# Optimization experiments

Measured on AMD Instinct MI355X. Metric: run time of the kernel, lower is better.

The kernel has to match this reference:

```python
import jax, jax.numpy as jnp
import numpy as np

B, S, D, H, E = 8, 4096, 1024, 2048, 8


def setup_inputs() -> dict:
    key = jax.random.key(0)
    ks = jax.random.split(key, 7)
    scale = 0.02
    return {
        "x": jax.random.normal(ks[0], (B, S, D), dtype=jnp.float32),
        "W1": jax.random.normal(ks[1], (E, D, H), dtype=jnp.float32) * scale,
        "b1": jnp.zeros((E, H), dtype=jnp.float32),
        "W2": jax.random.normal(ks[2], (E, H, D), dtype=jnp.float32) * scale,
        "b2": jnp.zeros((E, D), dtype=jnp.float32),
        "Wg": jax.random.normal(ks[3], (D, E), dtype=jnp.float32) * scale,
        "bg": jnp.zeros((E,), dtype=jnp.float32),
    }


def reference(x, W1, b1, W2, b2, Wg, bg):
    # Gating: softmax then top-1 (argmax) routing.
    logits = jnp.einsum("bsd,de->bse", x, Wg) + bg          # [B,S,E]
    probs = jax.nn.softmax(logits, axis=-1)                    # [B,S,E]
    top1 = jnp.argmax(probs, axis=-1)                          # [B,S] int

    out = jnp.zeros_like(x)
    # Fixed, small expert count: loop over experts (jit-friendly, no dynamic
    # shapes). coef zeros out tokens not routed to expert e, matching the
    # masked scatter in the original (unrouted positions stay 0 -> impossible
    # with top-1 over all experts, but semantics are identical).
    for e in range(E):
        coef = jnp.where(top1 == e, probs[..., e], 0.0)[..., None]  # [B,S,1]
        h = jax.nn.gelu(jnp.einsum("bsd,dh->bsh", x, W1[e]) + b1[e],
                        approximate=False)                      # exact GELU, torch default
        y = jnp.einsum("bsh,hd->bsd", h, W2[e]) + b2[e]
        out = out + coef * y
    return out
```

## Files before the change

kernel.cpp:

```cpp
#include <hip/hip_runtime.h>
#include <hip/hip_bf16.h>
#include <math.h>

#define NTOK 32768
#define DD   1024
#define HH   2048
#define EE   8

#define BM 256
#define BN 256
#define BK 64
#define MAXT2 144
#define NBLK 128

typedef __bf16 bf16x8 __attribute__((ext_vector_type(8)));
typedef __bf16 bf16x4 __attribute__((ext_vector_type(4)));
typedef float  f32x4  __attribute__((ext_vector_type(4)));

__device__ __forceinline__ void gload_lds16(const void* g, void* l) {
  __builtin_amdgcn_global_load_lds((__attribute__((address_space(1))) void*)(g),
                                   (__attribute__((address_space(3))) void*)(l),
                                   16, 0, 0);
}

__global__ __launch_bounds__(256) void k_gating(
    const float* __restrict__ x, const float* __restrict__ wg,
    const float* __restrict__ bg, int* __restrict__ eid,
    float* __restrict__ coef, __bf16* __restrict__ xbf)
{
  int lane = threadIdx.x & 63;
  int wave = threadIdx.x >> 6;
  int t0 = blockIdx.x * 8 + wave * 2;

  const float* xr0 = x + (size_t)t0 * DD;
  const float* xr1 = x + (size_t)(t0 + 1) * DD;
  double s0[8] = {}, s1[8] = {};
#pragma unroll
  for (int it = 0; it < 4; ++it) {
    int c0 = it * 256 + lane * 4;
    float4 xa = *(const float4*)(xr0 + c0);
    float4 xb = *(const float4*)(xr1 + c0);
    bf16x4 ca, cb;
#pragma unroll
    for (int j = 0; j < 4; ++j) { ca[j] = (__bf16)(&xa.x)[j]; cb[j] = (__bf16)(&xb.x)[j]; }
    *(bf16x4*)(xbf + (size_t)t0 * DD + c0) = ca;
    *(bf16x4*)(xbf + (size_t)(t0 + 1) * DD + c0) = cb;
    const float* w = wg + (size_t)c0 * EE;
#pragma unroll
    for (int j = 0; j < 4; ++j) {
      double fa = (double)(&xa.x)[j];
      double fb = (double)(&xb.x)[j];
#pragma unroll
      for (int e2 = 0; e2 < 8; ++e2) {
        double wv = (double)w[j * EE + e2];
        s0[e2] += fa * wv;
        s1[e2] += fb * wv;
      }
    }
  }

  int sel = lane & 1, sel2 = (lane >> 1) & 1, sel3 = (lane >> 2) & 1;
  int e = (lane & 1) * 4 + (lane & 2) + ((lane >> 2) & 1);
  double bge = (double)bg[e];

#pragma unroll
  for (int tk = 0; tk < 2; ++tk) {
    double* s = tk ? s1 : s0;
    double v4[4];
#pragma unroll
    for (int j = 0; j < 4; ++j) {
      double keep = sel ? s[4 + j] : s[j];
      double send = sel ? s[j] : s[4 + j];
      v4[j] = keep + __shfl_xor(send, 1, 64);
    }
    double v2[2];
#pragma unroll
    for (int j = 0; j < 2; ++j) {
      double keep = sel2 ? v4[2 + j] : v4[j];
      double send = sel2 ? v4[j] : v4[2 + j];
      v2[j] = keep + __shfl_xor(send, 2, 64);
    }
    double keep = sel3 ? v2[1] : v2[0];
    double send = sel3 ? v2[0] : v2[1];
    double tt = keep + __shfl_xor(send, 4, 64);
    tt += __shfl_xor(tt, 8, 64);
    tt += __shfl_xor(tt, 16, 64);
    tt += __shfl_xor(tt, 32, 64);
    double logit = tt + bge;
    double ml = logit; int me = e;
#pragma unroll
    for (int d2 = 1; d2 < 8; d2 <<= 1) {
      double ol = __shfl_xor(ml, d2, 64);
      int oe = __shfl_xor(me, d2, 64);
      if (ol > ml || (ol == ml && oe < me)) { ml = ol; me = oe; }
    }
    double se = exp(logit - ml);
#pragma unroll
    for (int d2 = 1; d2 < 8; d2 <<= 1) se += __shfl_xor(se, d2, 64);
    if (lane == 0) {
      eid[t0 + tk] = me;
      coef[t0 + tk] = (float)(1.0 / se);
    }
  }
}

__global__ __launch_bounds__(256) void k_hist(const int* __restrict__ eid,
                                              int* __restrict__ bhist) {
  __shared__ int h[EE];
  if (threadIdx.x < EE) h[threadIdx.x] = 0;
  __syncthreads();
  int t = blockIdx.x * 256 + threadIdx.x;
  atomicAdd(&h[eid[t]], 1);
  __syncthreads();
  if (threadIdx.x < EE) bhist[blockIdx.x * EE + threadIdx.x] = h[threadIdx.x];
}

__global__ void k_scan(const int* __restrict__ bhist, int* __restrict__ offs,
                       int* __restrict__ bbase, int2* __restrict__ tiles) {
  __shared__ int counts_s[EE];
  __shared__ int offs_s[EE + 1];
  int lane = threadIdx.x;
  if (lane < EE) {
    int sum = 0;
    for (int b = 0; b < NBLK; ++b) sum += bhist[b * EE + lane];
    counts_s[lane] = sum;
  }
  __syncthreads();
  if (lane == 0) {
    int a = 0;
    for (int e = 0; e < EE; ++e) { offs_s[e] = a; offs[e] = a; a += counts_s[e]; }
    offs_s[EE] = a; offs[EE] = a;
    int nt = 0;
    for (int e = 0; e < EE; ++e)
      for (int mt = 0; mt * BM < counts_s[e]; ++mt) tiles[nt++] = make_int2(e, mt);
    for (; nt < MAXT2; ++nt) tiles[nt] = make_int2(-1, 0);
  }
  __syncthreads();
  if (lane < EE) {
    int run = offs_s[lane];
    for (int b = 0; b < NBLK; ++b) {
      bbase[b * EE + lane] = run;
      run += bhist[b * EE + lane];
    }
  }
}

__global__ __launch_bounds__(256) void k_scatter(const int* __restrict__ eid,
                                                 const int* __restrict__ bbase,
                                                 int* __restrict__ idx) {
  __shared__ int cur[EE];
  if (threadIdx.x < EE) cur[threadIdx.x] = bbase[blockIdx.x * EE + threadIdx.x];
  __syncthreads();
  int t = blockIdx.x * 256 + threadIdx.x;
  int e = eid[t];
  int p = atomicAdd(&cur[e], 1);
  idx[p] = t;
}

__global__ __launch_bounds__(256) void k_transpose(
    const float* __restrict__ w, __bf16* __restrict__ wt, int R, int C)
{
  __shared__ float tile[32][33];
  int e = blockIdx.z;
  int c0 = blockIdx.x * 32, rb = blockIdx.y * 256;
  const float* we = w + (size_t)e * R * C;
  __bf16* wte = wt + (size_t)e * R * C;
  int tx = threadIdx.x & 31, ty = threadIdx.x >> 5;
  for (int s = 0; s < 8; ++s) {
    int r0 = rb + s * 32;
#pragma unroll
    for (int j = 0; j < 32; j += 8)
      tile[ty + j][tx] = we[(size_t)(r0 + ty + j) * C + (c0 + tx)];
    __syncthreads();
#pragma unroll
    for (int j = 0; j < 32; j += 8)
      wte[(size_t)(c0 + ty + j) * R + (r0 + tx)] = (__bf16)tile[tx][ty + j];
    __syncthreads();
  }
}

__global__ __launch_bounds__(512, 2) void k_gemm1(
    const __bf16* __restrict__ xbf, const __bf16* __restrict__ w1t,
    const float* __restrict__ b1, const int* __restrict__ idx,
    const int* __restrict__ offs, const int2* __restrict__ tiles,
    __bf16* __restrict__ hbuf)
{
  int2 te = tiles[blockIdx.x];
  int e = te.x;
  if (e < 0) return;
  int mt = te.y, nt = blockIdx.y;
  int off = offs[e], cnt = offs[e + 1] - off;
  int n0 = nt * BN;

  __shared__ __align__(16) char smem[131072];
  char* sA = smem;
  char* sB = smem + 65536;

  const int tid = threadIdx.x;
  const int lane = tid & 63;
  const int wid = tid >> 6;
  const int wr = wid >> 2, wc = wid & 3;
  const int lr = lane & 15, lk = lane >> 4;

  int tokr[4], srow[4], sch[4];
#pragma unroll
  for (int i = 0; i < 4; ++i) {
    int q = i * 512 + tid;
    int row = q >> 3;
    srow[i] = row;
    sch[i] = (q & 7) ^ (row & 7);
    int rl = mt * BM + row; if (rl >= cnt) rl = cnt - 1;
    tokr[i] = idx[off + rl];
  }
  const char* bsrc = (const char*)(w1t + ((size_t)e * HH + n0) * DD);

  f32x4 acc[8][4] = {};

#pragma unroll
  for (int i = 0; i < 4; ++i)
    gload_lds16((const char*)xbf + ((size_t)tokr[i] * DD) * 2 + sch[i] * 16,
                sA + (i * 512 + tid) * 16);
#pragma unroll
  for (int i = 0; i < 4; ++i)
    gload_lds16(bsrc + (size_t)srow[i] * (DD * 2) + sch[i] * 16,
                sB + (i * 512 + tid) * 16);
  __syncthreads();

  int cur = 0;
  for (int kt = 0; kt < DD / BK; ++kt) {
    if (kt + 1 < DD / BK) {
      int k0 = (kt + 1) * BK;
      char* dA = sA + (cur ^ 1) * 32768;
      char* dB = sB + (cur ^ 1) * 32768;
#pragma unroll
      for (int i = 0; i < 4; ++i)
        gload_lds16((const char*)xbf + ((size_t)tokr[i] * DD + k0) * 2 + sch[i] * 16,
                    dA + (i * 512 + tid) * 16);
#pragma unroll
      for (int i = 0; i < 4; ++i)
        gload_lds16(bsrc + (size_t)srow[i] * (DD * 2) + (size_t)k0 * 2 + sch[i] * 16,
                    dB + (i * 512 + tid) * 16);
    }
    __builtin_amdgcn_sched_barrier(0);
    const char* cAb = sA + cur * 32768;
    const char* cBb = sB + cur * 32768;
#pragma unroll
    for (int kk = 0; kk < 2; ++kk) {
      bf16x8 af[8], bf[4];
#pragma unroll
      for (int m = 0; m < 8; ++m) {
        int row = wr * 128 + m * 16 + lr;
        af[m] = *(const bf16x8*)(cAb + row * 128 + (((kk * 4 + lk) ^ (row & 7)) * 16));
      }
#pragma unroll
      for (int n = 0; n < 4; ++n) {
        int row = wc * 64 + n * 16 + lr;
        bf[n] = *(const bf16x8*)(cBb + row * 128 + (((kk * 4 + lk) ^ (row & 7)) * 16));
      }
      __builtin_amdgcn_s_setprio(1);
#pragma unroll
      for (int m = 0; m < 8; ++m)
#pragma unroll
        for (int n = 0; n < 4; ++n)
          acc[m][n] = __builtin_amdgcn_mfma_f32_16x16x32_bf16(af[m], bf[n], acc[m][n], 0, 0, 0);
      __builtin_amdgcn_s_setprio(0);
    }
    __syncthreads();
    cur ^= 1;
  }

#pragma unroll
  for (int m = 0; m < 8; ++m) {
    int rb = mt * BM + wr * 128 + m * 16 + lk * 4;
#pragma unroll
    for (int n = 0; n < 4; ++n) {
      int col = n0 + wc * 64 + n * 16 + lr;
      float bias = b1[e * HH + col];
#pragma unroll
      for (int j = 0; j < 4; ++j) {
        int r = rb + j;
        if (r < cnt) {
          float vv = acc[m][n][j] + bias;
          float g = 0.5f * vv * (1.0f + erff(vv * 0.70710678118654752f));
          hbuf[(size_t)(off + r) * HH + col] = (__bf16)g;
        }
      }
    }
  }
}

__global__ __launch_bounds__(512, 2) void k_gemm2(
    const __bf16* __restrict__ hbuf, const __bf16* __restrict__ w2t,
    const float* __restrict__ b2, const int* __restrict__ idx,
    const int* __restrict__ offs, const int2* __restrict__ tiles,
    const float* __restrict__ coef, float* __restrict__ out)
{
  int2 te = tiles[blockIdx.x];
  int e = te.x;
  if (e < 0) return;
  int mt = te.y, nt = blockIdx.y;
  int off = offs[e], cnt = offs[e + 1] - off;
  int n0 = nt * BN;

  __shared__ __align__(16) char smem[131072];
  char* sA = smem;
  char* sB = smem + 65536;

  const int tid = threadIdx.x;
  const int lane = tid & 63;
  const int wid = tid >> 6;
  const int wr = wid >> 2, wc = wid & 3;
  const int lr = lane & 15, lk = lane >> 4;

  int arow[4], srow[4], sch[4];
#pragma unroll
  for (int i = 0; i < 4; ++i) {
    int q = i * 512 + tid;
    int row = q >> 3;
    srow[i] = row;
    sch[i] = (q & 7) ^ (row & 7);
    int rl = mt * BM + row; if (rl >= cnt) rl = cnt - 1;
    arow[i] = off + rl;
  }
  const char* bsrc = (const char*)(w2t + ((size_t)e * DD + n0) * HH);

  f32x4 acc[8][4] = {};

#pragma unroll
  for (int i = 0; i < 4; ++i)
    gload_lds16((const char*)hbuf + ((size_t)arow[i] * HH) * 2 + sch[i] * 16,
                sA + (i * 512 + tid) * 16);
#pragma unroll
  for (int i = 0; i < 4; ++i)
    gload_lds16(bsrc + (size_t)srow[i] * (HH * 2) + sch[i] * 16,
                sB + (i * 512 + tid) * 16);
  __syncthreads();

  int cur = 0;
  for (int kt = 0; kt < HH / BK; ++kt) {
    if (kt + 1 < HH / BK) {
      int k0 = (kt + 1) * BK;
      char* dA = sA + (cur ^ 1) * 32768;
      char* dB = sB + (cur ^ 1) * 32768;
#pragma unroll
      for (int i = 0; i < 4; ++i)
        gload_lds16((const char*)hbuf + ((size_t)arow[i] * HH + k0) * 2 + sch[i] * 16,
                    dA + (i * 512 + tid) * 16);
#pragma unroll
      for (int i = 0; i < 4; ++i)
        gload_lds16(bsrc + (size_t)srow[i] * (HH * 2) + (size_t)k0 * 2 + sch[i] * 16,
                    dB + (i * 512 + tid) * 16);
    }
    __builtin_amdgcn_sched_barrier(0);
    const char* cAb = sA + cur * 32768;
    const char* cBb = sB + cur * 32768;
#pragma unroll
    for (int kk = 0; kk < 2; ++kk) {
      bf16x8 af[8], bf[4];
#pragma unroll
      for (int m = 0; m < 8; ++m) {
        int row = wr * 128 + m * 16 + lr;
        af[m] = *(const bf16x8*)(cAb + row * 128 + (((kk * 4 + lk) ^ (row & 7)) * 16));
      }
#pragma unroll
      for (int n = 0; n < 4; ++n) {
        int row = wc * 64 + n * 16 + lr;
        bf[n] = *(const bf16x8*)(cBb + row * 128 + (((kk * 4 + lk) ^ (row & 7)) * 16));
      }
      __builtin_amdgcn_s_setprio(1);
#pragma unroll
      for (int m = 0; m < 8; ++m)
#pragma unroll
        for (int n = 0; n < 4; ++n)
          acc[m][n] = __builtin_amdgcn_mfma_f32_16x16x32_bf16(af[m], bf[n], acc[m][n], 0, 0, 0);
      __builtin_amdgcn_s_setprio(0);
    }
    __syncthreads();
    cur ^= 1;
  }

#pragma unroll
  for (int m = 0; m < 8; ++m) {
    int rb = mt * BM + wr * 128 + m * 16 + lk * 4;
#pragma unroll
    for (int j = 0; j < 4; ++j) {
      int r = rb + j;
      if (r < cnt) {
        int t = idx[off + r];
        float cf = coef[t];
#pragma unroll
        for (int n = 0; n < 4; ++n) {
          int col = n0 + wc * 64 + n * 16 + lr;
          out[(size_t)t * DD + col] = cf * (acc[m][n][j] + b2[e * DD + col]);
        }
      }
    }
  }
}

extern "C" void kernel_launch(void* const* d_in, const int* in_sizes, int n_in,
                              void* d_out, int out_size, void* d_ws, size_t ws_size,
                              hipStream_t stream)
{
  const float* x  = (const float*)d_in[0];
  const float* W1 = (const float*)d_in[1];
  const float* b1 = (const float*)d_in[2];
  const float* W2 = (const float*)d_in[3];
  const float* b2 = (const float*)d_in[4];
  const float* Wg = (const float*)d_in[5];
  const float* bg = (const float*)d_in[6];
  float* out = (float*)d_out;

  char* ws = (char*)d_ws;
  size_t o = 0;
  int* offs   = (int*)(ws + o); o += 64;
  int2* tiles = (int2*)(ws + o); o += MAXT2 * 8;
  int* bhist  = (int*)(ws + o); o += NBLK * EE * 4;
  int* bbase  = (int*)(ws + o); o += NBLK * EE * 4;
  int* eid    = (int*)(ws + o); o += (size_t)NTOK * 4;
  float* coef = (float*)(ws + o); o += (size_t)NTOK * 4;
  int* idx    = (int*)(ws + o); o += (size_t)NTOK * 4;
  o = (o + 255) & ~(size_t)255;
  __bf16* xbf = (__bf16*)(ws + o); o += (size_t)NTOK * DD * 2;
  __bf16* w1t = (__bf16*)(ws + o); o += (size_t)EE * HH * DD * 2;
  __bf16* w2t = (__bf16*)(ws + o); o += (size_t)EE * DD * HH * 2;
  __bf16* hbuf = (__bf16*)(ws + o); o += (size_t)NTOK * HH * 2;

  k_gating<<<NTOK / 8, 256, 0, stream>>>(x, Wg, bg, eid, coef, xbf);
  k_hist<<<NBLK, 256, 0, stream>>>(eid, bhist);
  k_scan<<<1, 64, 0, stream>>>(bhist, offs, bbase, tiles);
  k_scatter<<<NBLK, 256, 0, stream>>>(eid, bbase, idx);
  k_transpose<<<dim3(HH / 32, DD / 256, EE), 256, 0, stream>>>(W1, w1t, DD, HH);
  k_transpose<<<dim3(DD / 32, HH / 256, EE), 256, 0, stream>>>(W2, w2t, HH, DD);
  k_gemm1<<<dim3(MAXT2, HH / BN), 512, 0, stream>>>(xbf, w1t, b1, idx, offs, tiles, hbuf);
  k_gemm2<<<dim3(MAXT2, DD / BN), 512, 0, stream>>>(hbuf, w2t, b2, idx, offs, tiles, coef, out);
}
```

Before: 876.6 us.

## Restructure MoE GEMM mainloops into a four-slot, finely interleaved load/MFMA pipeline

Replaces the double-buffered 64-wide K loop in both expert GEMMs with a shared mainloop. It stages 32-wide K halves into four LDS slots, interleaves global-to-LDS staging with half-tile MFMA groups, and uses explicit vmcnt waits and split barriers so loads overlap compute more deeply. It also changes the LDS swizzle for the 64-byte rows. Separately, the exact erff GELU is replaced with an Abramowitz-Stegun polynomial approximation using __expf, which is cheaper but slightly less accurate. The extra barriers and the hand-tuned wait counts add synchronisation cost and are fragile if the staging order changes.

```diff
diff --git a/kernel.cpp b/kernel.cpp
--- a/kernel.cpp
+++ b/kernel.cpp
@@ -21,6 +21,16 @@
   __builtin_amdgcn_global_load_lds((__attribute__((address_space(1))) void*)(g),
                                    (__attribute__((address_space(3))) void*)(l),
                                    16, 0, 0);
+}
+
+__device__ __forceinline__ float fast_gelu(float v) {
+  float az = fabsf(v) * 0.70710678118654752f;
+  float t = 1.0f / (1.0f + 0.3275911f * az);
+  float poly = t * (0.254829592f + t * (-0.284496736f +
+               t * (1.421413741f + t * (-1.453152027f + t * 1.061405429f))));
+  float erfa = 1.0f - poly * __expf(-az * az);
+  float s = copysignf(erfa, v);
+  return 0.5f * v * (1.0f + s);
 }
 
 __global__ __launch_bounds__(256) void k_gating(
@@ -179,6 +189,109 @@
   }
 }
 
+
+#define STAGE_A(u, kk, slot) do { \
+    gload_lds16(aSrc0 + (u) * 128 + (kk) * 64, sA + (slot) * 16384 + tid * 16); \
+    gload_lds16(aSrc1 + (u) * 128 + (kk) * 64, sA + (slot) * 16384 + 8192 + tid * 16); \
+  } while (0)
+#define STAGE_B(u, kk, slot) do { \
+    gload_lds16(bSrc0 + (u) * 128 + (kk) * 64, sB + (slot) * 16384 + tid * 16); \
+    gload_lds16(bSrc1 + (u) * 128 + (kk) * 64, sB + (slot) * 16384 + 8192 + tid * 16); \
+  } while (0)
+#define LDA4(slot, mq) do { \
+    const char* _b = sA + (slot) * 16384 + (mq) * 4096 + aoff; \
+    af[0] = *(const bf16x8*)(_b); \
+    af[1] = *(const bf16x8*)(_b + 1024); \
+    af[2] = *(const bf16x8*)(_b + 2048); \
+    af[3] = *(const bf16x8*)(_b + 3072); \
+  } while (0)
+#define LDB4(slot) do { \
+    const char* _b = sB + (slot) * 16384 + boff; \
+    bfr[0] = *(const bf16x8*)(_b); \
+    bfr[1] = *(const bf16x8*)(_b + 1024); \
+    bfr[2] = *(const bf16x8*)(_b + 2048); \
+    bfr[3] = *(const bf16x8*)(_b + 3072); \
+  } while (0)
+#define MM16(mq) do { \
+    __builtin_amdgcn_s_setprio(1); \
+    _Pragma("unroll") \
+    for (int _m = 0; _m < 4; ++_m) \
+      _Pragma("unroll") \
+      for (int _n = 0; _n < 4; ++_n) \
+        acc[(mq) * 4 + _m][_n] = __builtin_amdgcn_mfma_f32_16x16x32_bf16( \
+            af[_m], bfr[_n], acc[(mq) * 4 + _m][_n], 0, 0, 0); \
+    __builtin_amdgcn_s_setprio(0); \
+  } while (0)
+#define BAR_IN()  do { __builtin_amdgcn_s_barrier(); __builtin_amdgcn_sched_barrier(0); } while (0)
+#define BAR_OUT() do { __builtin_amdgcn_s_barrier(); } while (0)
+#define VM8()  asm volatile("s_waitcnt vmcnt(8)" ::: "memory")
+#define VM4()  asm volatile("s_waitcnt vmcnt(4)" ::: "memory")
+#define VM0()  asm volatile("s_waitcnt vmcnt(0)" ::: "memory")
+
+template <int NT>
+__device__ __forceinline__ void moe_mainloop(
+    const char* aSrc0, const char* aSrc1, const char* bSrc0, const char* bSrc1,
+    char* sA, char* sB, int tid, int aoff, int boff, f32x4 (&acc)[8][4])
+{
+  bf16x8 af[4], bfr[4];
+
+  STAGE_A(0, 0, 0); STAGE_B(0, 0, 0);
+  STAGE_A(0, 1, 1); STAGE_B(0, 1, 1);
+  STAGE_A(1, 0, 2); STAGE_B(1, 0, 2);
+  VM8();
+  BAR_OUT();
+
+  for (int t2 = 0; t2 < NT / 2 - 1; ++t2) {
+    const int u1 = 2 * t2 + 1, u2 = 2 * t2 + 2, u3 = 2 * t2 + 3;
+    LDA4(0, 0); LDB4(0);
+    STAGE_A(u1, 1, 3);
+    BAR_IN(); MM16(0); BAR_OUT();
+    LDA4(0, 1);
+    STAGE_B(u1, 1, 3);
+    BAR_IN(); MM16(1); VM8(); BAR_OUT();
+    LDA4(1, 0); LDB4(1);
+    STAGE_A(u2, 0, 0);
+    BAR_IN(); MM16(0); BAR_OUT();
+    LDA4(1, 1);
+    STAGE_B(u2, 0, 0);
+    BAR_IN(); MM16(1); VM8(); BAR_OUT();
+    LDA4(2, 0); LDB4(2);
+    STAGE_A(u2, 1, 1);
+    BAR_IN(); MM16(0); BAR_OUT();
+    LDA4(2, 1);
+    STAGE_B(u2, 1, 1);
+    BAR_IN(); MM16(1); VM8(); BAR_OUT();
+    LDA4(3, 0); LDB4(3);
+    STAGE_A(u3, 0, 2);
+    BAR_IN(); MM16(0); BAR_OUT();
+    LDA4(3, 1);
+    STAGE_B(u3, 0, 2);
+    BAR_IN(); MM16(1); VM8(); BAR_OUT();
+  }
+
+  {
+    const int u1 = NT - 1;
+    LDA4(0, 0); LDB4(0);
+    STAGE_A(u1, 1, 3);
+    BAR_IN(); MM16(0); BAR_OUT();
+    LDA4(0, 1);
+    STAGE_B(u1, 1, 3);
+    BAR_IN(); MM16(1); VM8(); BAR_OUT();
+    LDA4(1, 0); LDB4(1);
+    BAR_IN(); MM16(0); BAR_OUT();
+    LDA4(1, 1);
+    BAR_IN(); MM16(1); VM4(); BAR_OUT();
+    LDA4(2, 0); LDB4(2);
+    BAR_IN(); MM16(0); BAR_OUT();
+    LDA4(2, 1);
+    BAR_IN(); MM16(1); VM0(); BAR_OUT();
+    LDA4(3, 0); LDB4(3);
+    BAR_IN(); MM16(0); BAR_OUT();
+    LDA4(3, 1);
+    BAR_IN(); MM16(1);
+  }
+}
+
 __global__ __launch_bounds__(512, 2) void k_gemm1(
     const __bf16* __restrict__ xbf, const __bf16* __restrict__ w1t,
     const float* __restrict__ b1, const int* __restrict__ idx,
@@ -201,73 +314,22 @@
   const int wid = tid >> 6;
   const int wr = wid >> 2, wc = wid & 3;
   const int lr = lane & 15, lk = lane >> 4;
-
-  int tokr[4], srow[4], sch[4];
-#pragma unroll
-  for (int i = 0; i < 4; ++i) {
-    int q = i * 512 + tid;
-    int row = q >> 3;
-    srow[i] = row;
-    sch[i] = (q & 7) ^ (row & 7);
-    int rl = mt * BM + row; if (rl >= cnt) rl = cnt - 1;
-    tokr[i] = idx[off + rl];
-  }
-  const char* bsrc = (const char*)(w1t + ((size_t)e * HH + n0) * DD);
+  const int xorb = ((lr >> 3) & 1) << 1;
+  const int aoff = (wr * 128 + lr) * 64 + ((lk ^ xorb) * 16);
+  const int boff = (wc * 64 + lr) * 64 + ((lk ^ xorb) * 16);
+
+  int row0 = tid >> 2, row1 = (512 + tid) >> 2;
+  int g0 = (tid & 3) ^ (((row0 >> 3) & 1) << 1);
+  int g1 = ((512 + tid) & 3) ^ (((row1 >> 3) & 1) << 1);
+  int rl0 = mt * BM + row0; if (rl0 >= cnt) rl0 = cnt - 1;
+  int rl1 = mt * BM + row1; if (rl1 >= cnt) rl1 = cnt - 1;
+  const char* aSrc0 = (const char*)xbf + (size_t)idx[off + rl0] * (DD * 2) + g0 * 16;
+  const char* aSrc1 = (const char*)xbf + (size_t)idx[off + rl1] * (DD * 2) + g1 * 16;
+  const char* bSrc0 = (const char*)w1t + ((size_t)e * HH + n0 + row0) * (DD * 2) + g0 * 16;
+  const char* bSrc1 = (const char*)w1t + ((size_t)e * HH + n0 + row1) * (DD * 2) + g1 * 16;
 
   f32x4 acc[8][4] = {};
-
-#pragma unroll
-  for (int i = 0; i < 4; ++i)
-    gload_lds16((const char*)xbf + ((size_t)tokr[i] * DD) * 2 + sch[i] * 16,
-                sA + (i * 512 + tid) * 16);
-#pragma unroll
-  for (int i = 0; i < 4; ++i)
-    gload_lds16(bsrc + (size_t)srow[i] * (DD * 2) + sch[i] * 16,
-                sB + (i * 512 + tid) * 16);
-  __syncthreads();
-
-  int cur = 0;
-  for (int kt = 0; kt < DD / BK; ++kt) {
-    if (kt + 1 < DD / BK) {
-      int k0 = (kt + 1) * BK;
-      char* dA = sA + (cur ^ 1) * 32768;
-      char* dB = sB + (cur ^ 1) * 32768;
-#pragma unroll
-      for (int i = 0; i < 4; ++i)
-        gload_lds16((const char*)xbf + ((size_t)tokr[i] * DD + k0) * 2 + sch[i] * 16,
-                    dA + (i * 512 + tid) * 16);
-#pragma unroll
-      for (int i = 0; i < 4; ++i)
-        gload_lds16(bsrc + (size_t)srow[i] * (DD * 2) + (size_t)k0 * 2 + sch[i] * 16,
-                    dB + (i * 512 + tid) * 16);
-    }
-    __builtin_amdgcn_sched_barrier(0);
-    const char* cAb = sA + cur * 32768;
-    const char* cBb = sB + cur * 32768;
-#pragma unroll
-    for (int kk = 0; kk < 2; ++kk) {
-      bf16x8 af[8], bf[4];
-#pragma unroll
-      for (int m = 0; m < 8; ++m) {
-        int row = wr * 128 + m * 16 + lr;
-        af[m] = *(const bf16x8*)(cAb + row * 128 + (((kk * 4 + lk) ^ (row & 7)) * 16));
-      }
-#pragma unroll
-      for (int n = 0; n < 4; ++n) {
-        int row = wc * 64 + n * 16 + lr;
-        bf[n] = *(const bf16x8*)(cBb + row * 128 + (((kk * 4 + lk) ^ (row & 7)) * 16));
-      }
-      __builtin_amdgcn_s_setprio(1);
-#pragma unroll
-      for (int m = 0; m < 8; ++m)
-#pragma unroll
-        for (int n = 0; n < 4; ++n)
-          acc[m][n] = __builtin_amdgcn_mfma_f32_16x16x32_bf16(af[m], bf[n], acc[m][n], 0, 0, 0);
-      __builtin_amdgcn_s_setprio(0);
-    }
-    __syncthreads();
-    cur ^= 1;
-  }
+  moe_mainloop<DD / BK>(aSrc0, aSrc1, bSrc0, bSrc1, sA, sB, tid, aoff, boff, acc);
 
 #pragma unroll
   for (int m = 0; m < 8; ++m) {
@@ -279,11 +341,8 @@
 #pragma unroll
       for (int j = 0; j < 4; ++j) {
         int r = rb + j;
-        if (r < cnt) {
-          float vv = acc[m][n][j] + bias;
-          float g = 0.5f * vv * (1.0f + erff(vv * 0.70710678118654752f));
-          hbuf[(size_t)(off + r) * HH + col] = (__bf16)g;
-        }
+        if (r < cnt)
+          hbuf[(size_t)(off + r) * HH + col] = (__bf16)fast_gelu(acc[m][n][j] + bias);
       }
     }
   }
@@ -311,73 +370,22 @@
   const int wid = tid >> 6;
   const int wr = wid >> 2, wc = wid & 3;
   const int lr = lane & 15, lk = lane >> 4;
-
-  int arow[4], srow[4], sch[4];
-#pragma unroll
-  for (int i = 0; i < 4; ++i) {
-    int q = i * 512 + tid;
-    int row = q >> 3;
-    srow[i] = row;
-    sch[i] = (q & 7) ^ (row & 7);
-    int rl = mt * BM + row; if (rl >= cnt) rl = cnt - 1;
-    arow[i] = off + rl;
-  }
-  const char* bsrc = (const char*)(w2t + ((size_t)e * DD + n0) * HH);
+  const int xorb = ((lr >> 3) & 1) << 1;
+  const int aoff = (wr * 128 + lr) * 64 + ((lk ^ xorb) * 16);
+  const int boff = (wc * 64 + lr) * 64 + ((lk ^ xorb) * 16);
+
+  int row0 = tid >> 2, row1 = (512 + tid) >> 2;
+  int g0 = (tid & 3) ^ (((row0 >> 3) & 1) << 1);
+  int g1 = ((512 + tid) & 3) ^ (((row1 >> 3) & 1) << 1);
+  int rl0 = mt * BM + row0; if (rl0 >= cnt) rl0 = cnt - 1;
+  int rl1 = mt * BM + row1; if (rl1 >= cnt) rl1 = cnt - 1;
+  const char* aSrc0 = (const char*)hbuf + (size_t)(off + rl0) * (HH * 2) + g0 * 16;
+  const char* aSrc1 = (const char*)hbuf + (size_t)(off + rl1) * (HH * 2) + g1 * 16;
+  const char* bSrc0 = (const char*)w2t + ((size_t)e * DD + n0 + row0) * (HH * 2) + g0 * 16;
+  const char* bSrc1 = (const char*)w2t + ((size_t)e * DD + n0 + row1) * (HH * 2) + g1 * 16;
 
   f32x4 acc[8][4] = {};
-
-#pragma unroll
-  for (int i = 0; i < 4; ++i)
-    gload_lds16((const char*)hbuf + ((size_t)arow[i] * HH) * 2 + sch[i] * 16,
-                sA + (i * 512 + tid) * 16);
-#pragma unroll
-  for (int i = 0; i < 4; ++i)
-    gload_lds16(bsrc + (size_t)srow[i] * (HH * 2) + sch[i] * 16,
-                sB + (i * 512 + tid) * 16);
-  __syncthreads();
-
-  int cur = 0;
-  for (int kt = 0; kt < HH / BK; ++kt) {
-    if (kt + 1 < HH / BK) {
-      int k0 = (kt + 1) * BK;
-      char* dA = sA + (cur ^ 1) * 32768;
-      char* dB = sB + (cur ^ 1) * 32768;
-#pragma unroll
-      for (int i = 0; i < 4; ++i)
-        gload_lds16((const char*)hbuf + ((size_t)arow[i] * HH + k0) * 2 + sch[i] * 16,
-                    dA + (i * 512 + tid) * 16);
-#pragma unroll
-      for (int i = 0; i < 4; ++i)
-        gload_lds16(bsrc + (size_t)srow[i] * (HH * 2) + (size_t)k0 * 2 + sch[i] * 16,
-                    dB + (i * 512 + tid) * 16);
-    }
-    __builtin_amdgcn_sched_barrier(0);
-    const char* cAb = sA + cur * 32768;
-    const char* cBb = sB + cur * 32768;
-#pragma unroll
-    for (int kk = 0; kk < 2; ++kk) {
-      bf16x8 af[8], bf[4];
-#pragma unroll
-      for (int m = 0; m < 8; ++m) {
-        int row = wr * 128 + m * 16 + lr;
-        af[m] = *(const bf16x8*)(cAb + row * 128 + (((kk * 4 + lk) ^ (row & 7)) * 16));
-      }
-#pragma unroll
-      for (int n = 0; n < 4; ++n) {
-        int row = wc * 64 + n * 16 + lr;
-        bf[n] = *(const bf16x8*)(cBb + row * 128 + (((kk * 4 + lk) ^ (row & 7)) * 16));
-      }
-      __builtin_amdgcn_s_setprio(1);
-#pragma unroll
-      for (int m = 0; m < 8; ++m)
-#pragma unroll
-        for (int n = 0; n < 4; ++n)
-          acc[m][n] = __builtin_amdgcn_mfma_f32_16x16x32_bf16(af[m], bf[n], acc[m][n], 0, 0, 0);
-      __builtin_amdgcn_s_setprio(0);
-    }
-    __syncthreads();
-    cur ^= 1;
-  }
+  moe_mainloop<HH / BK>(aSrc0, aSrc1, bSrc0, bSrc1, sA, sB, tid, aoff, boff, acc);
 
 #pragma unroll
   for (int m = 0; m < 8; ++m) {
```

Result: no change. 889.9 us (+1.5%).
